# Performance work log

Hardware: AMD Instinct MI355X
Metric: run time of the kernel (lower is better)

Reference implementation:

```python
import math
import jax, jax.numpy as jnp
import numpy as np

# gpt-oss config constants (layer_idx=1 -> sliding_window disabled)
HID = 2880
N_HEADS = 64
N_KV = 8
D_HEAD = 64
GROUPS = N_HEADS // N_KV  # 8 query heads per kv head
SLIDING_WINDOW = 0        # layer_idx % 2 == 1 -> full causal attention
SM_SCALE = 1.0 / math.sqrt(D_HEAD)
EPS = 1e-5

ROPE_BASE = 150000.0
INIT_CTX = 4096
SCALING = 32.0
NTK_ALPHA = 1.0
NTK_BETA = 32.0


def _rope_cos_sin(num_tokens: int):
    """YaRN-scaled RoPE tables, fp32, positions 0..num_tokens-1 (offset=0, no cache)."""
    d_half = D_HEAD // 2
    freq = ROPE_BASE ** (np.arange(0, D_HEAD, 2, dtype=np.float64) / D_HEAD)
    concentration = 0.1 * math.log(SCALING) + 1.0
    low = d_half * math.log(INIT_CTX / (NTK_BETA * 2 * math.pi)) / math.log(ROPE_BASE)
    high = d_half * math.log(INIT_CTX / (NTK_ALPHA * 2 * math.pi)) / math.log(ROPE_BASE)
    interpolation = 1.0 / (SCALING * freq)
    extrapolation = 1.0 / freq
    ramp = (np.arange(d_half, dtype=np.float64) - low) / (high - low)
    mask = 1.0 - np.clip(ramp, 0.0, 1.0)
    inv_freq = interpolation * (1.0 - mask) + extrapolation * mask
    t = np.arange(num_tokens, dtype=np.float64)
    freqs = np.outer(t, inv_freq)  # [S, d_half]
    cos = (np.cos(freqs) * concentration).astype(np.float32)
    sin = (np.sin(freqs) * concentration).astype(np.float32)
    return jnp.asarray(cos), jnp.asarray(sin)


def _rotate(x, cos, sin):
    # x: [B, S, nh, D]; cos/sin: [S, D/2]
    c = cos[None, :, None, :]
    s = sin[None, :, None, :]
    x1, x2 = jnp.split(x, 2, axis=-1)
    return jnp.concatenate([x1 * c - x2 * s, x2 * c + x1 * s], axis=-1)


def setup_inputs() -> dict:
    key = jax.random.key(0)
    ks = jax.random.split(key, 5)
    B, S = 1, 1536
    x = jax.random.normal(ks[0], (B, S, HID), dtype=jnp.float32)
    sinks = jax.random.normal(ks[1], (N_HEADS,), dtype=jnp.float32) * 0.5
    norm_scale = jnp.ones((HID,), dtype=jnp.float32)
    qkv_dim = D_HEAD * (N_HEADS + 2 * N_KV)  # 5120
    qkv_w = jax.random.normal(ks[2], (qkv_dim, HID), dtype=jnp.float32) * 0.02
    qkv_b = jnp.zeros((qkv_dim,), dtype=jnp.float32)
    out_w = jax.random.normal(ks[3], (HID, N_HEADS * D_HEAD), dtype=jnp.float32) * 0.02
    out_b = jnp.zeros((HID,), dtype=jnp.float32)
    return {"x": x, "sinks": sinks, "norm_scale": norm_scale,
            "qkv_w": qkv_w, "qkv_b": qkv_b, "out_w": out_w, "out_b": out_b}


def reference(x, sinks, norm_scale, qkv_w, qkv_b, out_w, out_b):
    B, S, _ = x.shape
    # RMSNorm (fp32)
    t = x * jax.lax.rsqrt(jnp.mean(x * x, axis=-1, keepdims=True) + EPS) * norm_scale
    # fused QKV projection
    qkv = jnp.einsum('bsd,od->bso', t, qkv_w) + qkv_b
    q, k, v = jnp.split(qkv, [N_HEADS * D_HEAD, (N_HEADS + N_KV) * D_HEAD], axis=-1)
    q = q.reshape(B, S, N_HEADS, D_HEAD)
    k = k.reshape(B, S, N_KV, D_HEAD)
    v = v.reshape(B, S, N_KV, D_HEAD)
    # RoPE (offset = 0, no cache)
    cos, sin = _rope_cos_sin(S)
    q = _rotate(q, cos, sin)
    k = _rotate(k, cos, sin)
    # GQA: head h = g*N_KV + kv
    q = q.reshape(B, S, GROUPS, N_KV, D_HEAD)
    scores = jnp.einsum('bqgkd,bskd->bgkqs', q, k) * SM_SCALE  # [B,G,KV,S,S]
    i = jnp.arange(S)[:, None]
    j = jnp.arange(S)[None, :]
    allowed = j <= i  # causal
    if SLIDING_WINDOW > 0:
        allowed = allowed & (i - j < SLIDING_WINDOW)
    scores = jnp.where(allowed[None, None, None, :, :], scores, -1e30)
    # softmax with learned per-head sink logit in the denominator
    sink = sinks.reshape(GROUPS, N_KV)[None, :, :, None]  # [1,G,KV,1]
    m = jnp.maximum(jnp.max(scores, axis=-1), sink)       # [B,G,KV,S]
    p = jnp.exp(scores - m[..., None])
    denom = jnp.sum(p, axis=-1) + jnp.exp(sink - m)
    attn = p / denom[..., None]
    o = jnp.einsum('bgkqs,bskd->bqgkd', attn, v).reshape(B, S, N_HEADS * D_HEAD)
    y = jnp.einsum('bse,oe->bso', o, out_w) + out_b
    return x + y
```

## Files before the change

kernel.cpp:

```cpp
#include <hip/hip_runtime.h>
#include <hip/hip_bf16.h>
#include <math.h>

typedef unsigned short u16;
typedef __attribute__((ext_vector_type(8))) short bf16x8;
typedef __attribute__((ext_vector_type(4))) float f32x4;
typedef __attribute__((ext_vector_type(4))) u16 u16x4;

#define S_LEN   1536
#define HID     2880
#define NH      64
#define NKV     8
#define DH      64
#define QKV_N   5120
#define QDIM    4096
#define KVDIM   512
#define SMSCALE 0.125f
#define EPSV    1e-5f

__device__ __forceinline__ float b2f(u16 u) {
    unsigned int v = ((unsigned int)u) << 16;
    float f; __builtin_memcpy(&f, &v, 4); return f;
}
__device__ __forceinline__ u16 f2b(float f) {
    __hip_bfloat16 h = __float2bfloat16(f);
    return *reinterpret_cast<u16*>(&h);
}
__device__ __forceinline__ void gld16(const u16* g, u16* l) {
    __builtin_amdgcn_global_load_lds(
        (const __attribute__((address_space(1))) unsigned int*)g,
        (__attribute__((address_space(3))) unsigned int*)l, 16, 0, 0);
}
#define WAIT_VM6()   __builtin_amdgcn_s_waitcnt(0xF76)
#define WAIT_VM4()   __builtin_amdgcn_s_waitcnt(0xF74)
#define WAIT_VM0()   __builtin_amdgcn_s_waitcnt(0xF70)

__global__ __launch_bounds__(256) void conv_bf16_kernel(
    const float* __restrict__ src, u16* __restrict__ dst, int n4)
{
    int i = blockIdx.x * 256 + threadIdx.x;
    if (i >= n4) return;
    float4 v = ((const float4*)src)[i];
    u16x4 o;
    o.x = f2b(v.x); o.y = f2b(v.y); o.z = f2b(v.z); o.w = f2b(v.w);
    ((u16x4*)dst)[i] = o;
}

__global__ __launch_bounds__(256) void rmsnorm_kernel(
    const float* __restrict__ x, const float* __restrict__ ns, u16* __restrict__ t)
{
    const int s = blockIdx.x;
    const int tid = threadIdx.x;
    const float* xr = x + (size_t)s * HID;
    float ss = 0.f;
    for (int i = tid; i < HID; i += 256) { float v = xr[i]; ss += v * v; }
    for (int off = 32; off > 0; off >>= 1) ss += __shfl_down(ss, off);
    __shared__ float red[4];
    if ((tid & 63) == 0) red[tid >> 6] = ss;
    __syncthreads();
    float tot = red[0] + red[1] + red[2] + red[3];
    float scale = rsqrtf(tot / (float)HID + EPSV);
    u16* tr = t + (size_t)s * HID;
    for (int i = tid; i < HID; i += 256)
        tr[i] = f2b(xr[i] * scale * ns[i]);
}

__global__ __launch_bounds__(256) void rope_table_kernel(float* __restrict__ cosT, float* __restrict__ sinT)
{
    int idx = blockIdx.x * 256 + threadIdx.x;
    if (idx >= S_LEN * 32) return;
    int s = idx >> 5, i = idx & 31;
    const double PI2 = 6.283185307179586476925286766559;
    double base = 150000.0;
    double freq = pow(base, (double)(2 * i) / 64.0);
    double conc = 0.1 * log(32.0) + 1.0;
    double low  = 32.0 * log(4096.0 / (32.0 * PI2)) / log(base);
    double high = 32.0 * log(4096.0 / (1.0  * PI2)) / log(base);
    double interp = 1.0 / (32.0 * freq);
    double extrap = 1.0 / freq;
    double ramp = ((double)i - low) / (high - low);
    double msk = 1.0 - fmin(fmax(ramp, 0.0), 1.0);
    double invf = interp * (1.0 - msk) + extrap * msk;
    double ang = (double)s * invf;
    cosT[idx] = (float)(cos(ang) * conc);
    sinT[idx] = (float)(sin(ang) * conc);
}

__global__ __launch_bounds__(512, 2) void gemm_bt_8p_kernel(
    const u16* __restrict__ A, const u16* __restrict__ B,
    u16* __restrict__ Cp, u16* __restrict__ Cp2,
    int M, int N, int K, int it0, int it1, int ntm, int ntn)
{
    extern __shared__ __align__(16) u16 smem[];
    u16* sAp = smem;
    u16* sBp = smem + 32768;

    const int tid  = threadIdx.x;
    const int wave = tid >> 6, lane = tid & 63;
    const int quad = lane >> 4, l16 = lane & 15;
    const int wm = wave >> 2, wn = wave & 3;

    const int nwg  = gridDim.x;
    const int cpx  = nwg >> 3;
    const int flat = blockIdx.x;
    const int swz  = (flat & 7) * cpx + (flat >> 3);
    const int tpz  = ntm * ntn;
    const int z    = swz / tpz;
    const int rem  = swz - z * tpz;
    const int nt   = rem / ntm;
    const int mt   = rem - nt * ntm;
    const int bm = mt * 256, bn = nt * 256;
    const int niter = z ? it1 : it0;
    const int kb    = z ? (it0 + (z - 1) * it1) * 64 : 0;
    u16* C = (z < 2) ? (Cp + (size_t)z * M * N) : Cp2;

    const int r2  = tid >> 2;
    const int ks8 = (tid & 3) * 8;
    const u16* gA0 = A + (size_t)(bm + r2) * K + kb + ks8;
    const u16* gA1 = gA0 + (size_t)128 * K;
    int brA = bn + r2;       if (brA > N - 1) brA = N - 1;
    int brB = bn + 128 + r2; if (brB > N - 1) brB = N - 1;
    const u16* gB0 = B + (size_t)brA * K + kb + ks8;
    const u16* gB1 = B + (size_t)brB * K + kb + ks8;
    const int sw = wave * 512;

    f32x4 acc[8][4];
    #pragma unroll
    for (int i = 0; i < 8; i++)
        #pragma unroll
        for (int j = 0; j < 4; j++) acc[i][j] = (f32x4){0.f, 0.f, 0.f, 0.f};

    auto stA = [&](int c, int kh, int t) {
        u16* d = sAp + (((c << 1) | kh) << 13);
        const int koff = t * 64 + kh * 32;
        gld16(gA0 + koff, d + sw);
        gld16(gA1 + koff, d + 4096 + sw);
    };
    auto stB = [&](int c, int kh, int t) {
        u16* d = sBp + (((c << 1) | kh) << 13);
        const int koff = t * 64 + kh * 32;
        gld16(gB0 + koff, d + sw);
        gld16(gB1 + koff, d + 4096 + sw);
    };

    bf16x8 bv[4];
    const int arow = wm * 128 + l16;
    const int brow = wn * 64 + l16;
    auto rdB = [&](int c, int ks) {
        const u16* p = sBp + (((c << 1) | ks) << 13) + brow * 32 + quad * 8;
        #pragma unroll
        for (int nf = 0; nf < 4; nf++) bv[nf] = *(const bf16x8*)(p + nf * 16 * 32);
    };
    auto mmph = [&](int c, int ks, int mh) {
        const u16* p = sAp + (((c << 1) | ks) << 13) + (arow + mh * 64) * 32 + quad * 8;
        bf16x8 av[4];
        #pragma unroll
        for (int mf = 0; mf < 4; mf++) av[mf] = *(const bf16x8*)(p + mf * 16 * 32);
        __builtin_amdgcn_s_setprio(1);
        #pragma unroll
        for (int mf = 0; mf < 4; mf++)
            #pragma unroll
            for (int nf = 0; nf < 4; nf++)
                acc[mh * 4 + mf][nf] = __builtin_amdgcn_mfma_f32_16x16x32_bf16(
                    av[mf], bv[nf], acc[mh * 4 + mf][nf], 0, 0, 0);
        __builtin_amdgcn_s_setprio(0);
    };

    stA(0, 0, 0); stB(0, 0, 0); stA(0, 1, 0); stB(0, 1, 0);

    for (int t = 0; t < niter - 1; ++t) {
        const int c = t & 1;
        stA(c ^ 1, 0, t + 1);
        WAIT_VM6();
        __builtin_amdgcn_s_barrier();
        rdB(c, 0); mmph(c, 0, 0);
        stB(c ^ 1, 0, t + 1);
        mmph(c, 0, 1);
        stA(c ^ 1, 1, t + 1);
        WAIT_VM6();
        __builtin_amdgcn_s_barrier();
        rdB(c, 1); mmph(c, 1, 0);
        stB(c ^ 1, 1, t + 1);
        mmph(c, 1, 1);
    }
    {
        const int c = (niter - 1) & 1;
        WAIT_VM4();
        __builtin_amdgcn_s_barrier();
        rdB(c, 0); mmph(c, 0, 0); mmph(c, 0, 1);
        WAIT_VM0();
        __builtin_amdgcn_s_barrier();
        rdB(c, 1); mmph(c, 1, 0); mmph(c, 1, 1);
    }

    #pragma unroll
    for (int im = 0; im < 8; im++) {
        const int row0 = bm + wm * 128 + im * 16 + quad * 4;
        #pragma unroll
        for (int nf = 0; nf < 4; nf++) {
            const int col = bn + wn * 64 + nf * 16 + l16;
            if (col < N) {
                #pragma unroll
                for (int r = 0; r < 4; r++)
                    C[(size_t)(row0 + r) * N + col] = f2b(acc[im][nf][r]);
            }
        }
    }
}

__global__ __launch_bounds__(256) void rope_apply_kernel(
    const u16* __restrict__ p0, const u16* __restrict__ p1, const float* __restrict__ bias,
    const float* __restrict__ cosT, const float* __restrict__ sinT,
    u16* __restrict__ q_r, u16* __restrict__ k_r, u16* __restrict__ v_r)
{
    int idx = blockIdx.x * 256 + threadIdx.x;
    if (idx >= S_LEN * 80 * 64) return;
    int s  = idx / 5120;
    int rem = idx - s * 5120;
    int hh = rem >> 6;
    int i  = rem & 63;
    const u16* r0p = p0 + (size_t)s * QKV_N;
    const u16* r1p = p1 + (size_t)s * QKV_N;
    #define QKVV(o) (b2f(r0p[o]) + b2f(r1p[o]) + bias[o])
    if (hh < 64) {
        int off = hh * 64, j = i & 31;
        float x1 = QKVV(off + j), x2 = QKVV(off + 32 + j);
        float c = cosT[s * 32 + j], sn = sinT[s * 32 + j];
        float val = (i < 32) ? (x1 * c - x2 * sn) : (x2 * c + x1 * sn);
        q_r[(size_t)s * QDIM + off + i] = f2b(val * SMSCALE);
    } else if (hh < 72) {
        int kh = hh - 64, off = QDIM + kh * 64, j = i & 31;
        float x1 = QKVV(off + j), x2 = QKVV(off + 32 + j);
        float c = cosT[s * 32 + j], sn = sinT[s * 32 + j];
        float val = (i < 32) ? (x1 * c - x2 * sn) : (x2 * c + x1 * sn);
        k_r[(size_t)s * KVDIM + kh * 64 + i] = f2b(val);
    } else {
        int vh = hh - 72, off = QDIM + KVDIM + vh * 64;
        v_r[(size_t)s * KVDIM + vh * 64 + i] = f2b(QKVV(off + i));
    }
    #undef QKVV
}

__global__ __launch_bounds__(256) void vt_kernel(
    const u16* __restrict__ v_r, u16* __restrict__ vt)
{
    __shared__ u16 tile[64][72];
    const int s0 = blockIdx.x * 64;
    const int kvh = blockIdx.y;
    const int tid = threadIdx.x;
    const int r = tid >> 3;
    const int c = (tid & 7) * 8;

    #pragma unroll
    for (int rr = 0; rr < 64; rr += 32) {
        uint4 vv = *(const uint4*)(v_r + (size_t)(s0 + r + rr) * KVDIM + kvh * 64 + c);
        const u16* p = (const u16*)&vv;
        #pragma unroll
        for (int j = 0; j < 8; j++) tile[c + j][r + rr] = p[j];
    }
    __syncthreads();
    #pragma unroll
    for (int rr = 0; rr < 64; rr += 32) {
        uint4 ov;
        u16* p = (u16*)&ov;
        #pragma unroll
        for (int j = 0; j < 8; j++) p[j] = tile[r + rr][c + j];
        *(uint4*)(vt + (size_t)(kvh * 64 + r + rr) * S_LEN + s0 + c) = ov;
    }
}

__global__ __launch_bounds__(256) void attn_kernel(
    const u16* __restrict__ q_r, const u16* __restrict__ k_r, const u16* __restrict__ vt,
    const float* __restrict__ sinks, u16* __restrict__ o)
{
    __shared__ __align__(16) u16 sK[64 * 72];
    __shared__ __align__(16) u16 sVt[64 * 72];
    __shared__ __align__(16) u16 sP[4 * 16 * 72];

    const int bx = blockIdx.x, h = blockIdx.y;
    const int kvh = h & 7;
    const int tid = threadIdx.x, wave = tid >> 6, lane = tid & 63;
    const int quad = lane >> 4, l16 = lane & 15;
    const int srow = tid >> 3;
    const int scol = (tid & 7) * 8;
    u16* sPw = sP + wave * 16 * 72;
    const float sinkv = sinks[h];

    for (int phase = 0; phase < 2; ++phase) {
        const int qt = phase ? (23 - bx) : bx;
        const int q_i = qt * 64 + wave * 16 + l16;
        const u16* qp = q_r + (size_t)q_i * QDIM + h * 64 + quad * 8;
        bf16x8 aq0 = *(const bf16x8*)(qp);
        bf16x8 aq1 = *(const bf16x8*)(qp + 32);

        float m_i = sinkv, l_i = 1.0f;
        f32x4 acc[4];
        #pragma unroll
        for (int dt = 0; dt < 4; dt++) acc[dt] = (f32x4){0.f, 0.f, 0.f, 0.f};

        const int kend = qt * 64 + 64;
        for (int j0 = 0; j0 < kend; j0 += 64) {
            __syncthreads();
            #pragma unroll
            for (int rr = 0; rr < 64; rr += 32) {
                *(uint4*)(sK + (srow + rr) * 72 + scol) =
                    *(const uint4*)(k_r + (size_t)(j0 + srow + rr) * KVDIM + kvh * 64 + scol);
                *(uint4*)(sVt + (srow + rr) * 72 + scol) =
                    *(const uint4*)(vt + (size_t)(kvh * 64 + srow + rr) * S_LEN + j0 + scol);
            }
            __syncthreads();

            f32x4 sc[4];
            #pragma unroll
            for (int nt = 0; nt < 4; nt++) {
                const u16* kp = sK + (nt * 16 + l16) * 72 + quad * 8;
                bf16x8 bk0 = *(const bf16x8*)(kp);
                bf16x8 bk1 = *(const bf16x8*)(kp + 32);
                f32x4 s0 = (f32x4){0.f, 0.f, 0.f, 0.f};
                s0 = __builtin_amdgcn_mfma_f32_16x16x32_bf16(bk0, aq0, s0, 0, 0, 0);
                s0 = __builtin_amdgcn_mfma_f32_16x16x32_bf16(bk1, aq1, s0, 0, 0, 0);
                sc[nt] = s0;
            }

            if (j0 + 64 == kend) {
                #pragma unroll
                for (int nt = 0; nt < 4; nt++)
                    #pragma unroll
                    for (int r = 0; r < 4; r++)
                        if (j0 + nt * 16 + quad * 4 + r > q_i) sc[nt][r] = -INFINITY;
            }

            float vmax = sc[0][0];
            #pragma unroll
            for (int nt = 0; nt < 4; nt++)
                #pragma unroll
                for (int r = 0; r < 4; r++) vmax = fmaxf(vmax, sc[nt][r]);
            vmax = fmaxf(vmax, __shfl_xor(vmax, 16));
            vmax = fmaxf(vmax, __shfl_xor(vmax, 32));
            float mnew = fmaxf(m_i, vmax);
            float alpha = __expf(m_i - mnew);
            float ps = 0.f;
            u16x4 pk[4];
            #pragma unroll
            for (int nt = 0; nt < 4; nt++) {
                #pragma unroll
                for (int r = 0; r < 4; r++) {
                    float p = __expf(sc[nt][r] - mnew);
                    ps += p;
                    pk[nt][r] = f2b(p);
                }
            }
            ps += __shfl_xor(ps, 16);
            ps += __shfl_xor(ps, 32);
            l_i = l_i * alpha + ps;
            m_i = mnew;
            #pragma unroll
            for (int nt = 0; nt < 4; nt++)
                *(u16x4*)(sPw + l16 * 72 + nt * 16 + quad * 4) = pk[nt];
            #pragma unroll
            for (int dt = 0; dt < 4; dt++)
                #pragma unroll
                for (int r = 0; r < 4; r++) acc[dt][r] *= alpha;
            __threadfence_block();

            bf16x8 ap0 = *(const bf16x8*)(sPw + l16 * 72 + quad * 8);
            bf16x8 ap1 = *(const bf16x8*)(sPw + l16 * 72 + 32 + quad * 8);
            #pragma unroll
            for (int dt = 0; dt < 4; dt++) {
                const u16* vp = sVt + (dt * 16 + l16) * 72 + quad * 8;
                bf16x8 bv0 = *(const bf16x8*)(vp);
                bf16x8 bv1 = *(const bf16x8*)(vp + 32);
                acc[dt] = __builtin_amdgcn_mfma_f32_16x16x32_bf16(bv0, ap0, acc[dt], 0, 0, 0);
                acc[dt] = __builtin_amdgcn_mfma_f32_16x16x32_bf16(bv1, ap1, acc[dt], 0, 0, 0);
            }
        }

        float inv = 1.0f / l_i;
        #pragma unroll
        for (int dt = 0; dt < 4; dt++) {
            u16x4 ov;
            #pragma unroll
            for (int r = 0; r < 4; r++) ov[r] = f2b(acc[dt][r] * inv);
            *(u16x4*)(o + (size_t)q_i * QDIM + h * 64 + dt * 16 + quad * 4) = ov;
        }
    }
}

__global__ __launch_bounds__(256) void final_add_kernel(
    const u16* __restrict__ p0, const u16* __restrict__ p1, const u16* __restrict__ p2,
    const float* __restrict__ bias, const float* __restrict__ x, float* __restrict__ out)
{
    int i = blockIdx.x * 256 + threadIdx.x;
    int base = i * 4;
    int col = base % HID;
    float4 xo = *(const float4*)(x + base);
    float4 bi = *(const float4*)(bias + col);
    u16x4 a = ((const u16x4*)p0)[i];
    u16x4 b = ((const u16x4*)p1)[i];
    u16x4 c = ((const u16x4*)p2)[i];
    float4 r;
    r.x = b2f(a.x) + b2f(b.x) + b2f(c.x) + bi.x + xo.x;
    r.y = b2f(a.y) + b2f(b.y) + b2f(c.y) + bi.y + xo.y;
    r.z = b2f(a.z) + b2f(b.z) + b2f(c.z) + bi.z + xo.z;
    r.w = b2f(a.w) + b2f(b.w) + b2f(c.w) + bi.w + xo.w;
    *(float4*)(out + base) = r;
}

extern "C" void kernel_launch(void* const* d_in, const int* in_sizes, int n_in,
                              void* d_out, int out_size, void* d_ws, size_t ws_size,
                              hipStream_t stream)
{
    const float* x          = (const float*)d_in[0];
    const float* sinks      = (const float*)d_in[1];
    const float* norm_scale = (const float*)d_in[2];
    const float* qkv_w      = (const float*)d_in[3];
    const float* qkv_b      = (const float*)d_in[4];
    const float* out_w      = (const float*)d_in[5];
    const float* out_b      = (const float*)d_in[6];
    float* out = (float*)d_out;

    char* ws = (char*)d_ws;
    u16* t        = (u16*)(ws);
    u16* qkv_w_bf = (u16*)(ws + 8847360);
    u16* qkvp0    = (u16*)(ws + 38338560);
    u16* qkvp1    = (u16*)(ws + 54067200);
    float* cosT   = (float*)(ws + 69795840);
    float* sinT   = (float*)(ws + 69992448);
    u16* k_r      = (u16*)(ws);
    u16* vt       = (u16*)(ws + 1572864);
    u16* q_r      = (u16*)(ws + 3145728);
    u16* o        = (u16*)(ws + 15728640);
    u16* v_r      = (u16*)(ws + 28311552);
    u16* outp0    = (u16*)(ws + 28311552);
    u16* outp1    = (u16*)(ws + 37158912);
    u16* outp2    = (u16*)(ws + 3145728);
    u16* out_w_bf = (u16*)(ws + 46006272);

    static bool lds_attr_set = false;
    if (!lds_attr_set) {
        hipFuncSetAttribute(reinterpret_cast<const void*>(gemm_bt_8p_kernel),
                            hipFuncAttributeMaxDynamicSharedMemorySize, 131072);
        lds_attr_set = true;
    }

    rmsnorm_kernel<<<S_LEN, 256, 0, stream>>>(x, norm_scale, t);
    conv_bf16_kernel<<<(QKV_N * HID / 4 + 255) / 256, 256, 0, stream>>>(qkv_w, qkv_w_bf, QKV_N * HID / 4);
    rope_table_kernel<<<(S_LEN * 32) / 256, 256, 0, stream>>>(cosT, sinT);
    gemm_bt_8p_kernel<<<240, 512, 131072, stream>>>(
        t, qkv_w_bf, qkvp0, qkvp0, S_LEN, QKV_N, HID, 23, 22, 6, 20);
    rope_apply_kernel<<<(S_LEN * 80 * 64) / 256, 256, 0, stream>>>(
        qkvp0, qkvp1, qkv_b, cosT, sinT, q_r, k_r, v_r);
    vt_kernel<<<dim3(S_LEN / 64, NKV), 256, 0, stream>>>(v_r, vt);
    conv_bf16_kernel<<<(HID * QDIM / 4 + 255) / 256, 256, 0, stream>>>(out_w, out_w_bf, HID * QDIM / 4);
    attn_kernel<<<dim3(12, NH), 256, 0, stream>>>(q_r, k_r, vt, sinks, o);
    gemm_bt_8p_kernel<<<216, 512, 131072, stream>>>(
        o, out_w_bf, outp0, outp2, S_LEN, HID, QDIM, 22, 21, 6, 12);
    final_add_kernel<<<S_LEN * HID / 4 / 256, 256, 0, stream>>>(outp0, outp1, outp2, out_b, x, out);
}
```

Before: 335.4 us.

## Double-buffer K/V tiles in attention with register prefetch and lazy rescaling

Attention now keeps two LDS buffers for K and V^T and prefetches the next tile into registers while the current tile is being computed. This replaces two __syncthreads per iteration with a single barrier and hides global load latency. It also skips the online-softmax rescale unless the running max grows by more than 8, and raises wave priority around the MFMA blocks. The lazy rescale lets exp values exceed 1 (up to e^8) before bf16 rounding, and the single barrier reuse of the sP/sK buffers needs careful correctness checks.

```diff
diff --git a/kernel.cpp b/kernel.cpp
--- a/kernel.cpp
+++ b/kernel.cpp
@@ -34,6 +34,7 @@
 #define WAIT_VM6()   __builtin_amdgcn_s_waitcnt(0xF76)
 #define WAIT_VM4()   __builtin_amdgcn_s_waitcnt(0xF74)
 #define WAIT_VM0()   __builtin_amdgcn_s_waitcnt(0xF70)
+#define WAIT_LGKM0() __builtin_amdgcn_s_waitcnt(0xC07F)
 
 __global__ __launch_bounds__(256) void conv_bf16_kernel(
     const float* __restrict__ src, u16* __restrict__ dst, int n4)
@@ -273,8 +274,8 @@
     const u16* __restrict__ q_r, const u16* __restrict__ k_r, const u16* __restrict__ vt,
     const float* __restrict__ sinks, u16* __restrict__ o)
 {
-    __shared__ __align__(16) u16 sK[64 * 72];
-    __shared__ __align__(16) u16 sVt[64 * 72];
+    __shared__ __align__(16) u16 sK[2][64 * 72];
+    __shared__ __align__(16) u16 sVt[2][64 * 72];
     __shared__ __align__(16) u16 sP[4 * 16 * 72];
 
     const int bx = blockIdx.x, h = blockIdx.y;
@@ -286,6 +287,23 @@
     u16* sPw = sP + wave * 16 * 72;
     const float sinkv = sinks[h];
 
+    uint4 kreg0, kreg1, vreg0, vreg1;
+    const u16* kbase = k_r + (size_t)srow * KVDIM + kvh * 64 + scol;
+    const u16* vbase = vt + (size_t)(kvh * 64 + srow) * S_LEN + scol;
+
+    auto issue = [&](int j0) {
+        kreg0 = *(const uint4*)(kbase + (size_t)j0 * KVDIM);
+        kreg1 = *(const uint4*)(kbase + (size_t)(j0 + 32) * KVDIM);
+        vreg0 = *(const uint4*)(vbase + j0);
+        vreg1 = *(const uint4*)(vbase + (size_t)32 * S_LEN + j0);
+    };
+    auto lwrite = [&](int c) {
+        *(uint4*)(&sK[c][srow * 72 + scol])        = kreg0;
+        *(uint4*)(&sK[c][(srow + 32) * 72 + scol]) = kreg1;
+        *(uint4*)(&sVt[c][srow * 72 + scol])        = vreg0;
+        *(uint4*)(&sVt[c][(srow + 32) * 72 + scol]) = vreg1;
+    };
+
     for (int phase = 0; phase < 2; ++phase) {
         const int qt = phase ? (23 - bx) : bx;
         const int q_i = qt * 64 + wave * 16 + l16;
@@ -298,22 +316,22 @@
         #pragma unroll
         for (int dt = 0; dt < 4; dt++) acc[dt] = (f32x4){0.f, 0.f, 0.f, 0.f};
 
-        const int kend = qt * 64 + 64;
-        for (int j0 = 0; j0 < kend; j0 += 64) {
-            __syncthreads();
-            #pragma unroll
-            for (int rr = 0; rr < 64; rr += 32) {
-                *(uint4*)(sK + (srow + rr) * 72 + scol) =
-                    *(const uint4*)(k_r + (size_t)(j0 + srow + rr) * KVDIM + kvh * 64 + scol);
-                *(uint4*)(sVt + (srow + rr) * 72 + scol) =
-                    *(const uint4*)(vt + (size_t)(kvh * 64 + srow + rr) * S_LEN + j0 + scol);
-            }
-            __syncthreads();
+        const int ntile = qt + 1;
+        issue(0);
+        __syncthreads();
+
+        for (int tt = 0; tt < ntile; ++tt) {
+            const int c = tt & 1;
+            lwrite(c);
+            if (tt + 1 < ntile) issue((tt + 1) * 64);
+            WAIT_LGKM0();
+            __builtin_amdgcn_s_barrier();
 
             f32x4 sc[4];
+            __builtin_amdgcn_s_setprio(1);
             #pragma unroll
             for (int nt = 0; nt < 4; nt++) {
-                const u16* kp = sK + (nt * 16 + l16) * 72 + quad * 8;
+                const u16* kp = &sK[c][(nt * 16 + l16) * 72 + quad * 8];
                 bf16x8 bk0 = *(const bf16x8*)(kp);
                 bf16x8 bk1 = *(const bf16x8*)(kp + 32);
                 f32x4 s0 = (f32x4){0.f, 0.f, 0.f, 0.f};
@@ -321,13 +339,14 @@
                 s0 = __builtin_amdgcn_mfma_f32_16x16x32_bf16(bk1, aq1, s0, 0, 0, 0);
                 sc[nt] = s0;
             }
-
-            if (j0 + 64 == kend) {
+            __builtin_amdgcn_s_setprio(0);
+
+            if (tt == qt) {
                 #pragma unroll
                 for (int nt = 0; nt < 4; nt++)
                     #pragma unroll
                     for (int r = 0; r < 4; r++)
-                        if (j0 + nt * 16 + quad * 4 + r > q_i) sc[nt][r] = -INFINITY;
+                        if (tt * 64 + nt * 16 + quad * 4 + r > q_i) sc[nt][r] = -INFINITY;
             }
 
             float vmax = sc[0][0];
@@ -337,42 +356,47 @@
                 for (int r = 0; r < 4; r++) vmax = fmaxf(vmax, sc[nt][r]);
             vmax = fmaxf(vmax, __shfl_xor(vmax, 16));
             vmax = fmaxf(vmax, __shfl_xor(vmax, 32));
-            float mnew = fmaxf(m_i, vmax);
-            float alpha = __expf(m_i - mnew);
+            if (__any(vmax > m_i + 8.0f)) {
+                float mnew = fmaxf(m_i, vmax);
+                float alpha = __expf(m_i - mnew);
+                l_i *= alpha;
+                #pragma unroll
+                for (int dt = 0; dt < 4; dt++)
+                    #pragma unroll
+                    for (int r = 0; r < 4; r++) acc[dt][r] *= alpha;
+                m_i = mnew;
+            }
             float ps = 0.f;
             u16x4 pk[4];
             #pragma unroll
             for (int nt = 0; nt < 4; nt++) {
                 #pragma unroll
                 for (int r = 0; r < 4; r++) {
-                    float p = __expf(sc[nt][r] - mnew);
+                    float p = __expf(sc[nt][r] - m_i);
                     ps += p;
                     pk[nt][r] = f2b(p);
                 }
             }
             ps += __shfl_xor(ps, 16);
             ps += __shfl_xor(ps, 32);
-            l_i = l_i * alpha + ps;
-            m_i = mnew;
+            l_i += ps;
             #pragma unroll
             for (int nt = 0; nt < 4; nt++)
                 *(u16x4*)(sPw + l16 * 72 + nt * 16 + quad * 4) = pk[nt];
-            #pragma unroll
-            for (int dt = 0; dt < 4; dt++)
-                #pragma unroll
-                for (int r = 0; r < 4; r++) acc[dt][r] *= alpha;
             __threadfence_block();
 
             bf16x8 ap0 = *(const bf16x8*)(sPw + l16 * 72 + quad * 8);
             bf16x8 ap1 = *(const bf16x8*)(sPw + l16 * 72 + 32 + quad * 8);
+            __builtin_amdgcn_s_setprio(1);
             #pragma unroll
             for (int dt = 0; dt < 4; dt++) {
-                const u16* vp = sVt + (dt * 16 + l16) * 72 + quad * 8;
+                const u16* vp = &sVt[c][(dt * 16 + l16) * 72 + quad * 8];
                 bf16x8 bv0 = *(const bf16x8*)(vp);
                 bf16x8 bv1 = *(const bf16x8*)(vp + 32);
                 acc[dt] = __builtin_amdgcn_mfma_f32_16x16x32_bf16(bv0, ap0, acc[dt], 0, 0, 0);
                 acc[dt] = __builtin_amdgcn_mfma_f32_16x16x32_bf16(bv1, ap1, acc[dt], 0, 0, 0);
             }
+            __builtin_amdgcn_s_setprio(0);
         }
 
         float inv = 1.0f / l_i;
```

New measurement: 331.6 us. Within noise of the previous version (-1.1%).
